# Kernel tuning notes

Measured on AMD Instinct MI355X. Metric: run time of the kernel, lower is better.

The kernel has to match this reference:

```python
import jax, jax.numpy as jnp
import numpy as np

N = 524288   # total points across all scenes
B = 64       # number of scenes (segments)
C = 512      # in_dim (feature width)
H = C // 2   # hidden width of the score MLP
EPS = 1e-5   # torch LayerNorm default eps


def setup_inputs() -> dict:
    key = jax.random.key(0)
    ks = jax.random.split(key, 6)
    feats = jax.random.normal(ks[0], (N, C), jnp.float32)
    # ragged segment boundaries: B-1 distinct interior cut points -> no empty segments
    cuts = jnp.sort(jax.random.choice(ks[1], jnp.arange(1, N), (B - 1,), replace=False))
    offsets = jnp.concatenate([jnp.array([0], jnp.int32),
                               cuts.astype(jnp.int32),
                               jnp.array([N], jnp.int32)])
    ln_w = jnp.ones((C,), jnp.float32)
    ln_b = jnp.zeros((C,), jnp.float32)
    w1 = jax.random.normal(ks[2], (C, H), jnp.float32) * 0.02
    b1 = jnp.zeros((H,), jnp.float32)
    w2 = jax.random.normal(ks[3], (H,), jnp.float32) * 0.02
    b2 = jnp.zeros((1,), jnp.float32)
    return {"feats": feats, "ln_w": ln_w, "ln_b": ln_b,
            "w1": w1, "b1": b1, "w2": w2, "b2": b2, "offsets": offsets}


def reference(feats, ln_w, ln_b, w1, b1, w2, b2, offsets):
    # segment id of every point from the offset vector (vectorized, replaces the
    # per-scene Python loop in the original torch code)
    n = feats.shape[0]
    ids = jnp.searchsorted(offsets, jnp.arange(n, dtype=offsets.dtype), side='right') - 1

    # score MLP: LayerNorm -> Linear(C,H) -> GELU(exact) -> Linear(H,1)
    mu = feats.mean(axis=-1, keepdims=True)
    var = feats.var(axis=-1, keepdims=True)
    x = (feats - mu) * jax.lax.rsqrt(var + EPS) * ln_w + ln_b
    h = jax.nn.gelu(x @ w1 + b1, approximate=False)     # [N, H]
    s = h @ w2 + b2[0]                                  # [N] scalar score per point

    # segment softmax (numerically stable) then weighted sum per scene
    m = jax.ops.segment_max(s, ids, num_segments=B)     # [B]
    e = jnp.exp(s - m[ids])                             # [N]
    z = jax.ops.segment_sum(e, ids, num_segments=B)     # [B]
    w = e / z[ids]                                      # [N]
    pooled = jax.ops.segment_sum(feats * w[:, None], ids, num_segments=B)  # [B, C]
    return pooled
```

## Files before the change

kernel.cpp:

```cpp
#include <hip/hip_runtime.h>

#define NPTS 524288
#define NSEG 64

typedef __bf16 bf16x8 __attribute__((ext_vector_type(8)));
typedef float f32x4 __attribute__((ext_vector_type(4)));

__device__ __forceinline__ unsigned int f2bf(float f) {
  unsigned int u = __float_as_uint(f);
  return (u + 0x7FFFu + ((u >> 16) & 1u)) >> 16;
}

__global__ void prep_w1(const float* __restrict__ w1, unsigned short* __restrict__ w1p) {
  int idx = blockIdx.x * 256 + threadIdx.x;
  int k = idx >> 8, n = idx & 255;
  w1p[((k >> 3) << 11) + (n << 3) + (k & 7)] = (unsigned short)f2bf(w1[idx]);
}

__global__ void zero_out(float* __restrict__ out) {
  out[blockIdx.x * 256 + threadIdx.x] = 0.0f;
}

__global__ __launch_bounds__(256, 2) void score_kernel(
    const float* __restrict__ feats, const float* __restrict__ ln_w,
    const float* __restrict__ ln_b, const unsigned short* __restrict__ w1p,
    const float* __restrict__ b1, const float* __restrict__ w2,
    const float* __restrict__ b2, float* __restrict__ s_out) {
  __shared__ __align__(16) unsigned short xs[64 * 512];
  __shared__ float sred[4][64];
  char* xsb = (char*)xs;
  const int tid = threadIdx.x;
  const int lane = tid & 63;
  const int wid = tid >> 6;
  const long row0 = (long)blockIdx.x * 64;

  const int c0 = lane * 4;
  const float4 lw0 = *(const float4*)(ln_w + c0);
  const float4 lw1 = *(const float4*)(ln_w + 256 + c0);
  const float4 lb0 = *(const float4*)(ln_b + c0);
  const float4 lb1 = *(const float4*)(ln_b + 256 + c0);

  #pragma unroll 2
  for (int rr = 0; rr < 16; ++rr) {
    const int row = wid * 16 + rr;
    const float* rp = feats + (row0 + row) * 512;
    const float4 v0 = *(const float4*)(rp + c0);
    const float4 v1 = *(const float4*)(rp + 256 + c0);
    float sum = (v0.x + v0.y) + (v0.z + v0.w) + (v1.x + v1.y) + (v1.z + v1.w);
    float sq  = v0.x * v0.x + v0.y * v0.y + v0.z * v0.z + v0.w * v0.w
              + v1.x * v1.x + v1.y * v1.y + v1.z * v1.z + v1.w * v1.w;
    #pragma unroll
    for (int off = 32; off >= 1; off >>= 1) {
      sum += __shfl_xor(sum, off);
      sq  += __shfl_xor(sq, off);
    }
    const float mean = sum * (1.0f / 512.0f);
    const float var  = sq * (1.0f / 512.0f) - mean * mean;
    const float rstd = rsqrtf(var + 1e-5f);
    const float x0 = (v0.x - mean) * rstd * lw0.x + lb0.x;
    const float x1 = (v0.y - mean) * rstd * lw0.y + lb0.y;
    const float x2 = (v0.z - mean) * rstd * lw0.z + lb0.z;
    const float x3 = (v0.w - mean) * rstd * lw0.w + lb0.w;
    const float y0 = (v1.x - mean) * rstd * lw1.x + lb1.x;
    const float y1 = (v1.y - mean) * rstd * lw1.y + lb1.y;
    const float y2 = (v1.z - mean) * rstd * lw1.z + lb1.z;
    const float y3 = (v1.w - mean) * rstd * lw1.w + lb1.w;
    const unsigned int p0 = f2bf(x0) | (f2bf(x1) << 16);
    const unsigned int p1 = f2bf(x2) | (f2bf(x3) << 16);
    const unsigned int p2 = f2bf(y0) | (f2bf(y1) << 16);
    const unsigned int p3 = f2bf(y2) | (f2bf(y3) << 16);
    const unsigned int a0 = ((unsigned int)(row * 1024 + c0 * 2)) ^ (((unsigned int)(row & 7)) << 4);
    const unsigned int a1 = ((unsigned int)(row * 1024 + 512 + c0 * 2)) ^ (((unsigned int)(row & 7)) << 4);
    *(uint2*)(xsb + a0) = make_uint2(p0, p1);
    *(uint2*)(xsb + a1) = make_uint2(p2, p3);
  }
  __syncthreads();

  const int l15 = lane & 15, l4 = lane >> 4;
  const int nb = wid * 64;
  f32x4 acc[4][4];
  #pragma unroll
  for (int i = 0; i < 4; ++i)
    #pragma unroll
    for (int j = 0; j < 4; ++j)
      acc[i][j] = f32x4{0.f, 0.f, 0.f, 0.f};

  #pragma unroll 4
  for (int ks = 0; ks < 16; ++ks) {
    bf16x8 av[4], bv[4];
    #pragma unroll
    for (int mt = 0; mt < 4; ++mt) {
      const int row = mt * 16 + l15;
      const unsigned int ad =
          ((unsigned int)(row * 1024 + ks * 64 + l4 * 16)) ^ (((unsigned int)(row & 7)) << 4);
      av[mt] = *(const bf16x8*)(xsb + ad);
    }
    #pragma unroll
    for (int nt = 0; nt < 4; ++nt) {
      const int idx = (((ks * 4 + l4) << 8) + nb + nt * 16 + l15) << 3;
      bv[nt] = *(const bf16x8*)(w1p + idx);
    }
    #pragma unroll
    for (int mt = 0; mt < 4; ++mt)
      #pragma unroll
      for (int nt = 0; nt < 4; ++nt)
        acc[mt][nt] = __builtin_amdgcn_mfma_f32_16x16x32_bf16(av[mt], bv[nt], acc[mt][nt], 0, 0, 0);
  }

  float b1v[4], w2v[4];
  #pragma unroll
  for (int nt = 0; nt < 4; ++nt) {
    const int n = nb + nt * 16 + l15;
    b1v[nt] = b1[n];
    w2v[nt] = w2[n];
  }
  #pragma unroll
  for (int mt = 0; mt < 4; ++mt) {
    #pragma unroll
    for (int r = 0; r < 4; ++r) {
      float v = 0.0f;
      #pragma unroll
      for (int nt = 0; nt < 4; ++nt) {
        const float h = acc[mt][nt][r] + b1v[nt];
        const float g = 0.5f * h * (1.0f + erff(h * 0.70710678118654752f));
        v += g * w2v[nt];
      }
      v += __shfl_xor(v, 1);
      v += __shfl_xor(v, 2);
      v += __shfl_xor(v, 4);
      v += __shfl_xor(v, 8);
      if (l15 == 0) sred[wid][mt * 16 + l4 * 4 + r] = v;
    }
  }
  __syncthreads();
  if (tid < 64) {
    s_out[row0 + tid] = sred[0][tid] + sred[1][tid] + sred[2][tid] + sred[3][tid] + b2[0];
  }
}

__global__ void seg_stats(const float* __restrict__ s, const int* __restrict__ offs,
                          float* __restrict__ mz) {
  const int b = blockIdx.x;
  const int start = offs[b], end = offs[b + 1];
  const int tid = threadIdx.x;
  const int lane = tid & 63, wid = tid >> 6;
  __shared__ float red[4];

  float lm = -INFINITY;
  for (int i = start + tid; i < end; i += 256) lm = fmaxf(lm, s[i]);
  #pragma unroll
  for (int off = 32; off >= 1; off >>= 1) lm = fmaxf(lm, __shfl_xor(lm, off));
  if (lane == 0) red[wid] = lm;
  __syncthreads();
  const float m = fmaxf(fmaxf(red[0], red[1]), fmaxf(red[2], red[3]));
  __syncthreads();

  float ls = 0.0f;
  for (int i = start + tid; i < end; i += 256) ls += expf(s[i] - m);
  #pragma unroll
  for (int off = 32; off >= 1; off >>= 1) ls += __shfl_xor(ls, off);
  if (lane == 0) red[wid] = ls;
  __syncthreads();
  if (tid == 0) {
    const float z = red[0] + red[1] + red[2] + red[3];
    mz[b] = m;
    mz[NSEG + b] = 1.0f / z;
  }
}

__global__ __launch_bounds__(256) void pool_kernel(
    const float* __restrict__ feats, const float* __restrict__ s,
    const float* __restrict__ mz, const int* __restrict__ offs,
    float* __restrict__ out) {
  __shared__ int soffs[NSEG + 1];
  __shared__ float sm[NSEG], sz[NSEG];
  const int tid = threadIdx.x;
  if (tid < NSEG + 1) soffs[tid] = offs[tid];
  if (tid < NSEG) { sm[tid] = mz[tid]; sz[tid] = mz[NSEG + tid]; }
  __syncthreads();

  const int r0 = blockIdx.x * 256;
  int seg = 0;
  while (soffs[seg + 1] <= r0) ++seg;
  float m = sm[seg], iz = sz[seg];

  const float2* f2p = (const float2*)feats;
  float2 acc = make_float2(0.0f, 0.0f);
  float2 nxt = f2p[(size_t)r0 * 256 + tid];
  for (int r = r0; r < r0 + 256; ++r) {
    const float2 cur = nxt;
    if (r + 1 < NPTS) nxt = f2p[(size_t)(r + 1) * 256 + tid];
    if (r >= soffs[seg + 1]) {
      atomicAdd(&out[seg * 512 + tid * 2], acc.x);
      atomicAdd(&out[seg * 512 + tid * 2 + 1], acc.y);
      acc.x = 0.0f; acc.y = 0.0f;
      do { ++seg; } while (r >= soffs[seg + 1]);
      m = sm[seg]; iz = sz[seg];
    }
    const float wgt = expf(s[r] - m) * iz;
    acc.x += cur.x * wgt;
    acc.y += cur.y * wgt;
  }
  atomicAdd(&out[seg * 512 + tid * 2], acc.x);
  atomicAdd(&out[seg * 512 + tid * 2 + 1], acc.y);
}

extern "C" void kernel_launch(void* const* d_in, const int* in_sizes, int n_in,
                              void* d_out, int out_size, void* d_ws, size_t ws_size,
                              hipStream_t stream) {
  const float* feats = (const float*)d_in[0];
  const float* ln_w  = (const float*)d_in[1];
  const float* ln_b  = (const float*)d_in[2];
  const float* w1    = (const float*)d_in[3];
  const float* b1    = (const float*)d_in[4];
  const float* w2    = (const float*)d_in[5];
  const float* b2    = (const float*)d_in[6];
  const int* offs    = (const int*)d_in[7];
  float* out = (float*)d_out;

  char* ws = (char*)d_ws;
  float* s_buf = (float*)ws;
  float* mz    = (float*)(ws + (size_t)NPTS * 4);
  unsigned short* w1p = (unsigned short*)(ws + (size_t)NPTS * 4 + 4096);

  prep_w1<<<512, 256, 0, stream>>>(w1, w1p);
  zero_out<<<(NSEG * 512) / 256, 256, 0, stream>>>(out);
  score_kernel<<<NPTS / 64, 256, 0, stream>>>(feats, ln_w, ln_b, w1p, b1, w2, b2, s_buf);
  seg_stats<<<NSEG, 256, 0, stream>>>(s_buf, offs, mz);
  pool_kernel<<<NPTS / 256, 256, 0, stream>>>(feats, s_buf, mz, offs, out);
}
```

Measured before the change: 669.6 us.

## Fuse scoring with online per-block segment softmax partials and pooled sums

Merges score, segment stats and pooling into one kernel. Each 64-row block computes local per-segment max, exp-sum and weighted feature partials, re-reading its feats rows while they are likely still cache-resident. A small combine kernel then merges the partials per segment with log-sum-exp rescaling. This removes the second full pass over feats and the atomics, at the cost of a partials buffer. It also swaps erff for a polynomial erf approximation (Abramowitz-Stegun style), which adds a small approximation error.

```diff
diff --git a/kernel.cpp b/kernel.cpp
--- a/kernel.cpp
+++ b/kernel.cpp
@@ -2,6 +2,8 @@
 
 #define NPTS 524288
 #define NSEG 64
+#define NBLK (NPTS / 64)
+#define MAXP (NBLK + NSEG)
 
 typedef __bf16 bf16x8 __attribute__((ext_vector_type(8)));
 typedef float f32x4 __attribute__((ext_vector_type(4)));
@@ -9,6 +11,21 @@
 __device__ __forceinline__ unsigned int f2bf(float f) {
   unsigned int u = __float_as_uint(f);
   return (u + 0x7FFFu + ((u >> 16) & 1u)) >> 16;
+}
+
+__device__ __forceinline__ float gelu_f(float h) {
+  const float u = 0.70710678118654752f * h;
+  const float a = fabsf(u);
+  const float t = __builtin_amdgcn_rcpf(fmaf(0.3275911f, a, 1.0f));
+  const float e = __expf(-a * a);
+  float p = fmaf(1.061405429f, t, -1.453152027f);
+  p = fmaf(p, t, 1.421413741f);
+  p = fmaf(p, t, -0.284496736f);
+  p = fmaf(p, t, 0.254829592f);
+  p *= t;
+  const float erfa = fmaf(-p, e, 1.0f);
+  const float erfu = copysignf(erfa, u);
+  return 0.5f * h * (1.0f + erfu);
 }
 
 __global__ void prep_w1(const float* __restrict__ w1, unsigned short* __restrict__ w1p) {
@@ -17,30 +34,45 @@
   w1p[((k >> 3) << 11) + (n << 3) + (k & 7)] = (unsigned short)f2bf(w1[idx]);
 }
 
-__global__ void zero_out(float* __restrict__ out) {
-  out[blockIdx.x * 256 + threadIdx.x] = 0.0f;
-}
-
-__global__ __launch_bounds__(256, 2) void score_kernel(
+__global__ __launch_bounds__(256, 2) void fused_kernel(
     const float* __restrict__ feats, const float* __restrict__ ln_w,
     const float* __restrict__ ln_b, const unsigned short* __restrict__ w1p,
     const float* __restrict__ b1, const float* __restrict__ w2,
-    const float* __restrict__ b2, float* __restrict__ s_out) {
+    const float* __restrict__ b2, const int* __restrict__ offs,
+    float* __restrict__ m_arr, float* __restrict__ z_arr,
+    int* __restrict__ seg_arr, float* __restrict__ Pp) {
   __shared__ __align__(16) unsigned short xs[64 * 512];
   __shared__ float sred[4][64];
+  __shared__ float e_all[64];
+  __shared__ float sh_m[64];
+  __shared__ int sh_bound[66];
+  __shared__ int sh_meta[3];
   char* xsb = (char*)xs;
   const int tid = threadIdx.x;
   const int lane = tid & 63;
   const int wid = tid >> 6;
   const long row0 = (long)blockIdx.x * 64;
 
+  if (tid == 0) {
+    const int r0i = (int)row0;
+    int ncut = 0, pbase = blockIdx.x, seg0 = 0;
+    sh_bound[0] = 0;
+    for (int j = 1; j < NSEG; ++j) {
+      const int c = offs[j];
+      if (c <= r0i) { ++seg0; if (c & 63) ++pbase; }
+      else if (c < r0i + 64) { sh_bound[++ncut] = c - r0i; }
+    }
+    sh_bound[ncut + 1] = 64;
+    sh_meta[0] = ncut + 1; sh_meta[1] = pbase; sh_meta[2] = seg0;
+  }
+
   const int c0 = lane * 4;
   const float4 lw0 = *(const float4*)(ln_w + c0);
   const float4 lw1 = *(const float4*)(ln_w + 256 + c0);
   const float4 lb0 = *(const float4*)(ln_b + c0);
   const float4 lb1 = *(const float4*)(ln_b + 256 + c0);
 
-  #pragma unroll 2
+  #pragma unroll 4
   for (int rr = 0; rr < 16; ++rr) {
     const int row = wid * 16 + rr;
     const float* rp = feats + (row0 + row) * 512;
@@ -122,8 +154,7 @@
       #pragma unroll
       for (int nt = 0; nt < 4; ++nt) {
         const float h = acc[mt][nt][r] + b1v[nt];
-        const float g = 0.5f * h * (1.0f + erff(h * 0.70710678118654752f));
-        v += g * w2v[nt];
+        v += gelu_f(h) * w2v[nt];
       }
       v += __shfl_xor(v, 1);
       v += __shfl_xor(v, 2);
@@ -133,76 +164,102 @@
     }
   }
   __syncthreads();
-  if (tid < 64) {
-    s_out[row0 + tid] = sred[0][tid] + sred[1][tid] + sred[2][tid] + sred[3][tid] + b2[0];
-  }
-}
-
-__global__ void seg_stats(const float* __restrict__ s, const int* __restrict__ offs,
-                          float* __restrict__ mz) {
+
+  if (wid == 0) {
+    const int npart = sh_meta[0], pbase = sh_meta[1], seg0 = sh_meta[2];
+    const float sv = sred[0][lane] + sred[1][lane] + sred[2][lane] + sred[3][lane] + b2[0];
+    int pid = 0;
+    for (int i = 1; i < npart; ++i) pid += (sh_bound[i] <= lane) ? 1 : 0;
+    float mym = -INFINITY;
+    for (int k = 0; k < npart; ++k) {
+      float v = (pid == k) ? sv : -INFINITY;
+      #pragma unroll
+      for (int off = 32; off >= 1; off >>= 1) v = fmaxf(v, __shfl_xor(v, off));
+      if (pid == k) mym = v;
+      if (lane == 0) sh_m[k] = v;
+    }
+    const float e = __expf(sv - mym);
+    e_all[lane] = e;
+    for (int k = 0; k < npart; ++k) {
+      float v = (pid == k) ? e : 0.0f;
+      #pragma unroll
+      for (int off = 32; off >= 1; off >>= 1) v += __shfl_xor(v, off);
+      if (lane == 0) {
+        m_arr[pbase + k] = sh_m[k];
+        z_arr[pbase + k] = v;
+        seg_arr[pbase + k] = seg0 + k;
+      }
+    }
+  }
+  __syncthreads();
+
+  {
+    const int pbase = sh_meta[1];
+    const float2* f2p = (const float2*)feats + (size_t)row0 * 256;
+    float2* Pp2 = (float2*)Pp;
+    float2 pacc = make_float2(0.f, 0.f);
+    int k = 0;
+    #pragma unroll 4
+    for (int r = 0; r < 64; ++r) {
+      if (r == sh_bound[k + 1]) {
+        Pp2[(size_t)(pbase + k) * 256 + tid] = pacc;
+        pacc.x = 0.f; pacc.y = 0.f;
+        ++k;
+      }
+      const float e = e_all[r];
+      const float2 f = f2p[(size_t)r * 256 + tid];
+      pacc.x += e * f.x;
+      pacc.y += e * f.y;
+    }
+    Pp2[(size_t)(pbase + k) * 256 + tid] = pacc;
+  }
+}
+
+__global__ __launch_bounds__(512) void combine_kernel(
+    const int* __restrict__ offs, const float* __restrict__ m_arr,
+    const float* __restrict__ z_arr, const int* __restrict__ seg_arr,
+    const float* __restrict__ Pp, float* __restrict__ out) {
   const int b = blockIdx.x;
-  const int start = offs[b], end = offs[b + 1];
   const int tid = threadIdx.x;
   const int lane = tid & 63, wid = tid >> 6;
-  __shared__ float red[4];
+  __shared__ int s_lo, s_hi;
+  __shared__ float red[8];
+  __shared__ float s_MZ[2];
+
+  int Ptot = NBLK;
+  for (int j = 1; j < NSEG; ++j) Ptot += (offs[j] & 63) ? 1 : 0;
+
+  if (tid == 0) { s_lo = 1 << 30; s_hi = -1; }
+  __syncthreads();
+  int llo = 1 << 30, lhi = -1;
+  for (int p = tid; p < Ptot; p += 512) {
+    if (seg_arr[p] == b) { llo = min(llo, p); lhi = max(lhi, p); }
+  }
+  atomicMin(&s_lo, llo);
+  atomicMax(&s_hi, lhi);
+  __syncthreads();
+  const int lo = s_lo, hi = s_hi;
 
   float lm = -INFINITY;
-  for (int i = start + tid; i < end; i += 256) lm = fmaxf(lm, s[i]);
+  for (int p = lo + tid; p <= hi; p += 512) lm = fmaxf(lm, m_arr[p]);
   #pragma unroll
   for (int off = 32; off >= 1; off >>= 1) lm = fmaxf(lm, __shfl_xor(lm, off));
   if (lane == 0) red[wid] = lm;
   __syncthreads();
-  const float m = fmaxf(fmaxf(red[0], red[1]), fmaxf(red[2], red[3]));
-  __syncthreads();
-
-  float ls = 0.0f;
-  for (int i = start + tid; i < end; i += 256) ls += expf(s[i] - m);
-  #pragma unroll
-  for (int off = 32; off >= 1; off >>= 1) ls += __shfl_xor(ls, off);
-  if (lane == 0) red[wid] = ls;
-  __syncthreads();
   if (tid == 0) {
-    const float z = red[0] + red[1] + red[2] + red[3];
-    mz[b] = m;
-    mz[NSEG + b] = 1.0f / z;
-  }
-}
-
-__global__ __launch_bounds__(256) void pool_kernel(
-    const float* __restrict__ feats, const float* __restrict__ s,
-    const float* __restrict__ mz, const int* __restrict__ offs,
-    float* __restrict__ out) {
-  __shared__ int soffs[NSEG + 1];
-  __shared__ float sm[NSEG], sz[NSEG];
-  const int tid = threadIdx.x;
-  if (tid < NSEG + 1) soffs[tid] = offs[tid];
-  if (tid < NSEG) { sm[tid] = mz[tid]; sz[tid] = mz[NSEG + tid]; }
-  __syncthreads();
-
-  const int r0 = blockIdx.x * 256;
-  int seg = 0;
-  while (soffs[seg + 1] <= r0) ++seg;
-  float m = sm[seg], iz = sz[seg];
-
-  const float2* f2p = (const float2*)feats;
-  float2 acc = make_float2(0.0f, 0.0f);
-  float2 nxt = f2p[(size_t)r0 * 256 + tid];
-  for (int r = r0; r < r0 + 256; ++r) {
-    const float2 cur = nxt;
-    if (r + 1 < NPTS) nxt = f2p[(size_t)(r + 1) * 256 + tid];
-    if (r >= soffs[seg + 1]) {
-      atomicAdd(&out[seg * 512 + tid * 2], acc.x);
-      atomicAdd(&out[seg * 512 + tid * 2 + 1], acc.y);
-      acc.x = 0.0f; acc.y = 0.0f;
-      do { ++seg; } while (r >= soffs[seg + 1]);
-      m = sm[seg]; iz = sz[seg];
-    }
-    const float wgt = expf(s[r] - m) * iz;
-    acc.x += cur.x * wgt;
-    acc.y += cur.y * wgt;
-  }
-  atomicAdd(&out[seg * 512 + tid * 2], acc.x);
-  atomicAdd(&out[seg * 512 + tid * 2 + 1], acc.y);
+    float M = red[0];
+    for (int w = 1; w < 8; ++w) M = fmaxf(M, red[w]);
+    float Z = 0.0f;
+    for (int p = lo; p <= hi; ++p) Z += z_arr[p] * __expf(m_arr[p] - M);
+    s_MZ[0] = M; s_MZ[1] = Z;
+  }
+  __syncthreads();
+  const float M = s_MZ[0];
+  const float invZ = 1.0f / s_MZ[1];
+  float acc = 0.0f;
+  for (int p = lo; p <= hi; ++p)
+    acc += __expf(m_arr[p] - M) * Pp[(size_t)p * 512 + tid];
+  out[b * 512 + tid] = acc * invZ;
 }
 
 extern "C" void kernel_launch(void* const* d_in, const int* in_sizes, int n_in,
@@ -219,13 +276,14 @@
   float* out = (float*)d_out;
 
   char* ws = (char*)d_ws;
-  float* s_buf = (float*)ws;
-  float* mz    = (float*)(ws + (size_t)NPTS * 4);
-  unsigned short* w1p = (unsigned short*)(ws + (size_t)NPTS * 4 + 4096);
+  unsigned short* w1p = (unsigned short*)(ws);
+  float* m_arr  = (float*)(ws + 262144);
+  float* z_arr  = (float*)(ws + 327680);
+  int*   seg_arr= (int*)  (ws + 393216);
+  float* Pp     = (float*)(ws + 524288);
 
   prep_w1<<<512, 256, 0, stream>>>(w1, w1p);
-  zero_out<<<(NSEG * 512) / 256, 256, 0, stream>>>(out);
-  score_kernel<<<NPTS / 64, 256, 0, stream>>>(feats, ln_w, ln_b, w1p, b1, w2, b2, s_buf);
-  seg_stats<<<NSEG, 256, 0, stream>>>(s_buf, offs, mz);
-  pool_kernel<<<NPTS / 256, 256, 0, stream>>>(feats, s_buf, mz, offs, out);
-}
+  fused_kernel<<<NBLK, 256, 0, stream>>>(feats, ln_w, ln_b, w1p, b1, w2, b2, offs,
+                                         m_arr, z_arr, seg_arr, Pp);
+  combine_kernel<<<NSEG, 512, 0, stream>>>(offs, m_arr, z_arr, seg_arr, Pp, out);
+}
```

New measurement: 1.055 ms. 57.6% more time.
